# Kernel tuning notes

Hardware: AMD Instinct MI355X
Metric: run time of the kernel (lower is better)

The kernel has to match this reference:

```python
import jax, jax.numpy as jnp
import numpy as np


def _skew(p):
    # p: (...,3) -> (...,3,3) skew-symmetric matrices
    x, y, z = p[..., 0], p[..., 1], p[..., 2]
    o = jnp.zeros_like(x)
    return jnp.stack([
        jnp.stack([o, -z, y], -1),
        jnp.stack([z, o, -x], -1),
        jnp.stack([-y, x, o], -1)], -2)


def _so3exp(w):
    # Rodrigues formula for a single (3,) rotation vector
    theta = jnp.linalg.norm(w)
    small = theta < 1e-7
    th = jnp.where(small, 1.0, theta)
    W = _skew(w)
    A = jnp.where(small, 1.0, jnp.sin(th) / th)
    B = jnp.where(small, 0.5, (1.0 - jnp.cos(th)) / (th * th))
    return jnp.eye(3, dtype=w.dtype) + A * W + B * (W @ W)


def setup_inputs() -> dict:
    key = jax.random.key(0)
    k1, k2, k3, k4, k5, k6 = jax.random.split(key, 6)
    N, C, H, W = 100000, 128, 480, 640
    xy = jax.random.uniform(k1, (N, 2), minval=-1.0, maxval=1.0)
    z = jax.random.uniform(k2, (N, 1), minval=4.0, maxval=8.0)
    pts3D = jnp.concatenate([xy, z], -1).astype(jnp.float32)
    feature_ref = jax.random.normal(k3, (N, C), dtype=jnp.float32)
    feature_map_query = jax.random.normal(k4, (C, H, W), dtype=jnp.float32)
    feature_grad_x = jax.random.normal(k5, (C, H, W), dtype=jnp.float32) * 0.1
    feature_grad_y = jax.random.normal(k6, (C, H, W), dtype=jnp.float32) * 0.1
    K = jnp.array([[400.0, 0.0, 320.0], [0.0, 400.0, 200.0], [0.0, 0.0, 1.0]], dtype=jnp.float32)
    return {"pts3D": pts3D, "feature_ref": feature_ref,
            "feature_map_query": feature_map_query,
            "feature_grad_x": feature_grad_x, "feature_grad_y": feature_grad_y,
            "K": K, "n_iters": 5}


def reference(pts3D, feature_ref, feature_map_query, feature_grad_x, feature_grad_y, K, n_iters):
    C, H, W = feature_map_query.shape
    N = pts3D.shape[0]

    def gather(fm, ii, jj):
        return fm[:, ii, jj].T  # (N, C)

    def project(Rm, tv):
        p = pts3D @ Rm.T + tv                       # (N,3) points in camera frame
        uv = p @ K.T
        proj = jnp.round(uv[:, :2] / uv[:, 2:3]).astype(jnp.int32) - 1  # (N,2) [x,y]
        ii = jnp.clip(proj[:, 1], 0, H - 1)          # row (flip)
        jj = jnp.clip(proj[:, 0], 0, W - 1)          # col
        return p, ii, jj

    def step(carry, i):
        R, t, lam, lr, prev_cost = carry
        p, ii, jj = project(R, t)
        error = gather(feature_map_query, ii, jj) - feature_ref  # (N,C)
        cost_mean = (0.5 * (error ** 2).sum(-1)).mean()
        prev_cost = jnp.where(i == 0, cost_mean, prev_cost)
        eye = jnp.broadcast_to(jnp.eye(3, dtype=p.dtype), (N, 3, 3))
        J_p_T = jnp.concatenate([eye, -_skew(p)], -1)            # (N,3,6)
        fx, fy = K[0, 0], K[1, 1]
        x, y, z = p[:, 0], p[:, 1], p[:, 2]
        o = jnp.ones_like(z); zz = jnp.zeros_like(z)
        J_px_p = jnp.stack([fx * o, zz, -fx * x / z, zz, fy * o, -fy * y / z], -1)
        J_px_p = J_px_p.reshape(N, 2, 3) / z[:, None, None]       # (N,2,3)
        gx = gather(feature_grad_x, ii, jj)
        gy = gather(feature_grad_y, ii, jj)
        J_f_px = jnp.stack([gx, gy], -1)                          # (N,C,2)
        J = jnp.einsum('ncp,npq,nqk->nck', J_f_px, J_px_p, J_p_T)  # (N,C,6)
        g = jnp.einsum('nck,nc->k', J, error)                     # (6,)
        Hess = jnp.einsum('nci,ncj->ij', J, J)                    # (6,6)
        Hd = Hess + jnp.diag(jnp.diagonal(Hess) + 1e-9) * lam     # LM damping
        delta = -lr * jnp.linalg.solve(Hd, g)
        dt, dw = delta[:3], delta[3:6]
        dR = _so3exp(dw)
        R_new = dR @ R
        t_new = dR @ t + dt
        _, ii2, jj2 = project(R_new, t_new)
        new_error = gather(feature_map_query, ii2, jj2) - feature_ref
        new_cost = (0.5 * (new_error ** 2).sum(-1)).mean()
        worse = new_cost > prev_cost
        lam = jnp.clip(lam * jnp.where(worse, 10.0, 0.1), 1e-6, 1e4)
        lr = jnp.where(worse, jnp.clip(0.1 * lr, 1e-3, 1.0), 0.1)
        R = jnp.where(worse, R, R_new)
        t = jnp.where(worse, t, t_new)
        prev_cost = jnp.where(worse, prev_cost, new_cost)
        return (R, t, lam, lr, prev_cost), None

    R0 = jnp.eye(3, dtype=pts3D.dtype)
    t0 = jnp.array([1.0, 1.0, 0.0], dtype=pts3D.dtype)
    init = (R0, t0, jnp.float32(0.01), jnp.float32(0.1), jnp.float32(0.0))
    (R, t, _, _, _), _ = jax.lax.scan(step, init, jnp.arange(n_iters))
    return R, t
```

## Files before the change

### kernel.cpp

```cpp
#include <hip/hip_runtime.h>

#define NPTS 100000
#define CCH  128
#define HIMG 480
#define WIMG 640
#define HWSZ (HIMG*WIMG)
#define TROW 384
#define NSLOT 8

struct State {
  double slotsA[NSLOT][28];
  double slotsC[NSLOT][28];
  double accA[28];
  double accB;
  double prev_cost;
  float R[9];
  float t[3];
  float Rc[9];
  float tc[3];
  float lam;
  float lr;
};

__device__ State g_st;

#define HIDX(i,j) (6 + (6*(i)) - ((i)*((i)-1))/2 + ((j)-(i)))

__device__ __forceinline__ float sel6(int k, float a0,float a1,float a2,float a3,float a4,float a5){
  float r = a0;
  r = (k==1)?a1:r; r = (k==2)?a2:r; r = (k==3)?a3:r; r = (k==4)?a4:r; r = (k==5)?a5:r;
  return r;
}

#define TP_PIX 32
#define NTILE (HWSZ/TP_PIX)
#define TIX(p,c) ((p)*132 + ((c) ^ ((((p)>>2)&3)<<3)))

__global__ __launch_bounds__(256) void k_transpose(
    const float* __restrict__ Q, const float* __restrict__ GX,
    const float* __restrict__ GY, float* __restrict__ T)
{
  if(blockIdx.x==0 && threadIdx.x==0){
    for(int s=0;s<NSLOT;s++) for(int k=0;k<28;k++){ g_st.slotsA[s][k]=0.0; g_st.slotsC[s][k]=0.0; }
    g_st.prev_cost=0.0;
    g_st.R[0]=1.f; g_st.R[1]=0.f; g_st.R[2]=0.f;
    g_st.R[3]=0.f; g_st.R[4]=1.f; g_st.R[5]=0.f;
    g_st.R[6]=0.f; g_st.R[7]=0.f; g_st.R[8]=1.f;
    g_st.t[0]=1.f; g_st.t[1]=1.f; g_st.t[2]=0.f;
    g_st.lam=0.01f; g_st.lr=0.1f;
  }

  __shared__ float tile[TP_PIX*132];
  const int bid = blockIdx.x;
  const int m   = bid / NTILE;
  const int tl  = bid - m*NTILE;
  const int pbase = tl*TP_PIX;
  const float* __restrict__ src = (m==0)?Q:((m==1)?GX:GY);
  const int t = threadIdx.x;

  const int c_lo = t>>3;
  const int p4   = (t&7)<<2;
  #pragma unroll
  for(int k=0;k<4;k++){
    const int c = c_lo + 32*k;
    const float4 v = *reinterpret_cast<const float4*>(src + (size_t)c*HWSZ + pbase + p4);
    tile[TIX(p4+0,c)] = v.x;
    tile[TIX(p4+1,c)] = v.y;
    tile[TIX(p4+2,c)] = v.z;
    tile[TIX(p4+3,c)] = v.w;
  }
  __syncthreads();
  const int p = t>>3;
  const int a = t&7;
  float* dstp = T + (size_t)(pbase+p)*TROW + m*128;
  #pragma unroll
  for(int q=0;q<4;q++){
    const int ch = a*4 + 32*q;
    const float4 v = *reinterpret_cast<const float4*>(&tile[TIX(p,ch)]);
    *reinterpret_cast<float4*>(dstp + ch) = v;
  }
}

__global__ __launch_bounds__(256) void k_pass(
    const float* __restrict__ pts, const float* __restrict__ ref,
    const float* __restrict__ T,   const float* __restrict__ Kin, int cand)
{
  __shared__ double wacc[4][28];
  const int lane = threadIdx.x & 63;
  const int wid  = threadIdx.x >> 6;

  const float fx=Kin[0], cx=Kin[2], fy=Kin[4], cy=Kin[5];
  const float* Rp = cand ? g_st.Rc : g_st.R;
  const float* tp = cand ? g_st.tc : g_st.t;
  const float R00=Rp[0],R01=Rp[1],R02=Rp[2];
  const float R10=Rp[3],R11=Rp[4],R12=Rp[5];
  const float R20=Rp[6],R21=Rp[7],R22=Rp[8];
  const float t0=tp[0],t1=tp[1],t2=tp[2];

  float a[28];
  #pragma unroll
  for(int k=0;k<28;k++) a[k]=0.f;

  const int c0 = lane*2;
  const int wstride = gridDim.x*4;
  for(int n = blockIdx.x*4 + wid; n < NPTS; n += wstride){
    const float X=pts[3*n], Y=pts[3*n+1], Z=pts[3*n+2];
    const float x = R00*X + R01*Y + R02*Z + t0;
    const float y = R10*X + R11*Y + R12*Z + t1;
    const float z = R20*X + R21*Y + R22*Z + t2;
    const float uu = fx*x + cx*z;
    const float vv = fy*y + cy*z;
    const int pjx = (int)rintf(uu/z) - 1;
    const int pjy = (int)rintf(vv/z) - 1;
    const int jj = pjx<0?0:(pjx>(WIMG-1)?(WIMG-1):pjx);
    const int ii = pjy<0?0:(pjy>(HIMG-1)?(HIMG-1):pjy);
    const int idx = ii*WIMG + jj;

    const float* base = T + (size_t)idx*TROW + c0;
    const float2 qq = *reinterpret_cast<const float2*>(base);
    const float2 gg = *reinterpret_cast<const float2*>(base + 128);
    const float2 hh = *reinterpret_cast<const float2*>(base + 256);
    const float2 rr = *reinterpret_cast<const float2*>(ref + n*CCH + c0);
    const float e0 = qq.x-rr.x, e1 = qq.y-rr.y;

    const float see = e0*e0 + e1*e1;
    const float sb1 = gg.x*e0 + gg.y*e1;
    const float sb2 = hh.x*e0 + hh.y*e1;
    const float sa11= gg.x*gg.x + gg.y*gg.y;
    const float sa12= gg.x*hh.x + gg.y*hh.y;
    const float sa22= hh.x*hh.x + hh.y*hh.y;

    const float iz = 1.0f/z;
    const float ux = x*iz, vy = y*iz;
    float M0[6], M1[6];
    M0[0]=fx*iz; M0[1]=0.f;   M0[2]=-fx*ux*iz; M0[3]=-fx*ux*vy;       M0[4]=fx*(1.f+ux*ux); M0[5]=-fx*vy;
    M1[0]=0.f;   M1[1]=fy*iz; M1[2]=-fy*vy*iz; M1[3]=-fy*(1.f+vy*vy); M1[4]=fy*ux*vy;       M1[5]=fy*ux;

    #pragma unroll
    for(int i=0;i<6;i++) a[i] += M0[i]*sb1 + M1[i]*sb2;
    #pragma unroll
    for(int i=0;i<6;i++){
      #pragma unroll
      for(int j=i;j<6;j++){
        a[HIDX(i,j)] += sa11*(M0[i]*M0[j]) + sa12*(M0[i]*M1[j]+M1[i]*M0[j]) + sa22*(M1[i]*M1[j]);
      }
    }
    a[27] += see;
  }

  #pragma unroll
  for(int k=0;k<28;k++){
    double v = (double)a[k];
    #pragma unroll
    for(int m=1;m<64;m<<=1) v += __shfl_xor(v,m);
    if(lane==0) wacc[wid][k]=v;
  }
  __syncthreads();
  if(threadIdx.x<28){
    double s = wacc[0][threadIdx.x]+wacc[1][threadIdx.x]+wacc[2][threadIdx.x]+wacc[3][threadIdx.x];
    double* slot = cand ? g_st.slotsC[blockIdx.x & (NSLOT-1)] : g_st.slotsA[blockIdx.x & (NSLOT-1)];
    atomicAdd(&slot[threadIdx.x], s);
  }
}

__global__ void k_step(int iter){
  __shared__ double red[28];
  __shared__ double sC[28];
  const int t = threadIdx.x;
  if(t<28){
    double c=0.0, aa=0.0;
    for(int s=0;s<NSLOT;s++){ c += g_st.slotsC[s][t]; aa += g_st.slotsA[s][t]; }
    sC[t]=c; red[t]=aa;
  }
  __syncthreads();
  if(t!=0) return;

  if(iter>0){
    const double new_cost = 0.5*sC[27]/(double)NPTS;
    const bool worse = new_cost > g_st.prev_cost;
    float lam = g_st.lam * (worse?10.0f:0.1f);
    g_st.lam = fminf(fmaxf(lam,1e-6f),10000.0f);
    g_st.lr  = worse ? fminf(fmaxf(0.1f*g_st.lr,0.001f),1.0f) : 0.1f;
    if(!worse){
      for(int k=0;k<28;k++){
        red[k]=sC[k];
        g_st.slotsA[0][k]=sC[k];
        for(int s=1;s<NSLOT;s++) g_st.slotsA[s][k]=0.0;
      }
      for(int i=0;i<9;i++) g_st.R[i]=g_st.Rc[i];
      for(int i=0;i<3;i++) g_st.t[i]=g_st.tc[i];
      g_st.prev_cost = new_cost;
    }
    for(int s=0;s<NSLOT;s++) for(int k=0;k<28;k++) g_st.slotsC[s][k]=0.0;
  } else {
    g_st.prev_cost = 0.5*red[27]/(double)NPTS;
  }

  const double lam = (double)g_st.lam;
  double Hm[6][6];
  int m=0;
  for(int i=0;i<6;i++) for(int j=i;j<6;j++){ double v=red[6+m]; m++; Hm[i][j]=v; Hm[j][i]=v; }
  double A[6][7];
  for(int i=0;i<6;i++){
    for(int j=0;j<6;j++) A[i][j]=Hm[i][j];
    A[i][i] = Hm[i][i] + lam*(Hm[i][i]+1e-9);
    A[i][6] = red[i];
  }
  for(int k=0;k<6;k++){
    int piv=k; double mx=fabs(A[k][k]);
    for(int r=k+1;r<6;r++){ double v=fabs(A[r][k]); if(v>mx){mx=v;piv=r;} }
    if(piv!=k){ for(int c=k;c<7;c++){ double tmp=A[k][c]; A[k][c]=A[piv][c]; A[piv][c]=tmp; } }
    const double inv = 1.0/A[k][k];
    for(int r=k+1;r<6;r++){
      const double f = A[r][k]*inv;
      for(int c=k;c<7;c++) A[r][c] -= f*A[k][c];
    }
  }
  double xsol[6];
  for(int r=5;r>=0;r--){
    double s=A[r][6];
    for(int c=r+1;c<6;c++) s -= A[r][c]*xsol[c];
    xsol[r]=s/A[r][r];
  }
  const double lr = (double)g_st.lr;
  float d[6];
  for(int k=0;k<6;k++) d[k] = (float)(-lr*xsol[k]);

  const float wx=d[3], wy=d[4], wz=d[5];
  const float th2 = wx*wx+wy*wy+wz*wz;
  const float theta = sqrtf(th2);
  const bool small = theta < 1e-7f;
  const float th = small?1.0f:theta;
  const float Aa = small?1.0f:(sinf(th)/th);
  const float Bb = small?0.5f:((1.0f-cosf(th))/(th*th));
  float Wm[3][3] = {{0.f,-wz,wy},{wz,0.f,-wx},{-wy,wx,0.f}};
  float W2[3][3];
  for(int i=0;i<3;i++) for(int j=0;j<3;j++)
    W2[i][j] = Wm[i][0]*Wm[0][j] + Wm[i][1]*Wm[1][j] + Wm[i][2]*Wm[2][j];
  float dR[3][3];
  for(int i=0;i<3;i++) for(int j=0;j<3;j++)
    dR[i][j] = (i==j?1.f:0.f) + Aa*Wm[i][j] + Bb*W2[i][j];

  float Rn[9], tn[3];
  for(int i=0;i<3;i++){
    for(int j=0;j<3;j++)
      Rn[i*3+j] = dR[i][0]*g_st.R[0*3+j] + dR[i][1]*g_st.R[1*3+j] + dR[i][2]*g_st.R[2*3+j];
    tn[i] = dR[i][0]*g_st.t[0] + dR[i][1]*g_st.t[1] + dR[i][2]*g_st.t[2] + d[i];
  }
  for(int i=0;i<9;i++) g_st.Rc[i]=Rn[i];
  for(int i=0;i<3;i++) g_st.tc[i]=tn[i];
}

__global__ void k_finish(float* __restrict__ out, int out_size){
  const int t = threadIdx.x;
  if(t==0){
    double c=0.0; for(int s=0;s<NSLOT;s++) c += g_st.slotsC[s][27];
    const double new_cost = 0.5*c/(double)NPTS;
    if(!(new_cost > g_st.prev_cost)){
      for(int i=0;i<9;i++) g_st.R[i]=g_st.Rc[i];
      for(int i=0;i<3;i++) g_st.t[i]=g_st.tc[i];
    }
  }
  __syncthreads();
  if(t<9 && t<out_size) out[t]=g_st.R[t];
  else if(t<12 && t<out_size) out[t]=g_st.t[t-9];
}

__global__ void k_init(){
  if(threadIdx.x==0){
    for(int i=0;i<28;i++) g_st.accA[i]=0.0;
    g_st.accB=0.0; g_st.prev_cost=0.0;
    g_st.R[0]=1.f; g_st.R[1]=0.f; g_st.R[2]=0.f;
    g_st.R[3]=0.f; g_st.R[4]=1.f; g_st.R[5]=0.f;
    g_st.R[6]=0.f; g_st.R[7]=0.f; g_st.R[8]=1.f;
    g_st.t[0]=1.f; g_st.t[1]=1.f; g_st.t[2]=0.f;
    g_st.lam=0.01f; g_st.lr=0.1f;
  }
}

__global__ __launch_bounds__(256) void k_accum(
    const float* __restrict__ pts, const float* __restrict__ ref,
    const float* __restrict__ Q,   const float* __restrict__ GX,
    const float* __restrict__ GY,  const float* __restrict__ Kin)
{
  __shared__ double wacc[4][28];
  const int lane = threadIdx.x & 63;
  const int wid  = threadIdx.x >> 6;

  const float fx=Kin[0], cx=Kin[2], fy=Kin[4], cy=Kin[5];
  const float R00=g_st.R[0],R01=g_st.R[1],R02=g_st.R[2];
  const float R10=g_st.R[3],R11=g_st.R[4],R12=g_st.R[5];
  const float R20=g_st.R[6],R21=g_st.R[7],R22=g_st.R[8];
  const float t0=g_st.t[0],t1=g_st.t[1],t2=g_st.t[2];

  int role = 3, ci = 0, cj = 0;
  if(lane < 6){ role = 0; ci = lane; cj = lane; }
  else if(lane < 27){
    role = 1;
    const int tt = lane - 6;
    int i = 5;
    i = (tt < 20) ? 4 : i;
    i = (tt < 18) ? 3 : i;
    i = (tt < 15) ? 2 : i;
    i = (tt < 11) ? 1 : i;
    i = (tt <  6) ? 0 : i;
    const int rs = (i==0)?0:(i==1)?6:(i==2)?11:(i==3)?15:(i==4)?18:20;
    ci = i; cj = i + (tt - rs);
  }
  else if(lane == 27){ role = 2; }

  double acc = 0.0;
  const int c0 = lane*2;
  const int wstride = gridDim.x*4;
  for(int n = blockIdx.x*4 + wid; n < NPTS; n += wstride){
    const float X=pts[3*n], Y=pts[3*n+1], Z=pts[3*n+2];
    const float x = R00*X + R01*Y + R02*Z + t0;
    const float y = R10*X + R11*Y + R12*Z + t1;
    const float z = R20*X + R21*Y + R22*Z + t2;
    const float uu = fx*x + cx*z;
    const float vv = fy*y + cy*z;
    const int pjx = (int)rintf(uu/z) - 1;
    const int pjy = (int)rintf(vv/z) - 1;
    const int jj = pjx<0?0:(pjx>(WIMG-1)?(WIMG-1):pjx);
    const int ii = pjy<0?0:(pjy>(HIMG-1)?(HIMG-1):pjy);
    const int idx = ii*WIMG + jj;

    const int o0 = c0*HWSZ + idx;
    const float q0 = Q[o0],  q1 = Q[o0+HWSZ];
    const float gx0= GX[o0], gx1= GX[o0+HWSZ];
    const float gy0= GY[o0], gy1= GY[o0+HWSZ];
    const float2 rr = *reinterpret_cast<const float2*>(ref + n*CCH + c0);
    const float e0 = q0-rr.x, e1 = q1-rr.y;

    float see = e0*e0 + e1*e1;
    float sb1 = gx0*e0 + gx1*e1;
    float sb2 = gy0*e0 + gy1*e1;
    float sa11= gx0*gx0 + gx1*gx1;
    float sa12= gx0*gy0 + gx1*gy1;
    float sa22= gy0*gy0 + gy1*gy1;
    #pragma unroll
    for(int m=1;m<64;m<<=1){
      see += __shfl_xor(see,m);
      sb1 += __shfl_xor(sb1,m);
      sb2 += __shfl_xor(sb2,m);
      sa11+= __shfl_xor(sa11,m);
      sa12+= __shfl_xor(sa12,m);
      sa22+= __shfl_xor(sa22,m);
    }

    const float iz = 1.0f/z;
    const float ux = x*iz, vy = y*iz;
    const float m00=fx*iz, m01=0.f,    m02=-fx*ux*iz, m03=-fx*ux*vy,       m04=fx*(1.f+ux*ux), m05=-fx*vy;
    const float m10=0.f,   m11=fy*iz,  m12=-fy*vy*iz, m13=-fy*(1.f+vy*vy), m14=fy*ux*vy,       m15=fy*ux;

    float contrib;
    if(role==0){
      const float M0=sel6(ci,m00,m01,m02,m03,m04,m05);
      const float M1=sel6(ci,m10,m11,m12,m13,m14,m15);
      contrib = M0*sb1 + M1*sb2;
    } else if(role==1){
      const float M0i=sel6(ci,m00,m01,m02,m03,m04,m05);
      const float M1i=sel6(ci,m10,m11,m12,m13,m14,m15);
      const float M0j=sel6(cj,m00,m01,m02,m03,m04,m05);
      const float M1j=sel6(cj,m10,m11,m12,m13,m14,m15);
      contrib = sa11*(M0i*M0j) + sa12*(M0i*M1j + M1i*M0j) + sa22*(M1i*M1j);
    } else if(role==2){
      contrib = see;
    } else {
      contrib = 0.f;
    }
    acc += (double)contrib;
  }

  if(lane<28) wacc[wid][lane] = acc;
  __syncthreads();
  if(threadIdx.x<28){
    double s = wacc[0][threadIdx.x]+wacc[1][threadIdx.x]+wacc[2][threadIdx.x]+wacc[3][threadIdx.x];
    atomicAdd(&g_st.accA[threadIdx.x], s);
  }
}

__global__ __launch_bounds__(256) void k_cost(
    const float* __restrict__ pts, const float* __restrict__ ref,
    const float* __restrict__ Q,   const float* __restrict__ Kin)
{
  __shared__ double wacc[4];
  const int lane = threadIdx.x & 63;
  const int wid  = threadIdx.x >> 6;

  const float fx=Kin[0], cx=Kin[2], fy=Kin[4], cy=Kin[5];
  const float R00=g_st.Rc[0],R01=g_st.Rc[1],R02=g_st.Rc[2];
  const float R10=g_st.Rc[3],R11=g_st.Rc[4],R12=g_st.Rc[5];
  const float R20=g_st.Rc[6],R21=g_st.Rc[7],R22=g_st.Rc[8];
  const float t0=g_st.tc[0],t1=g_st.tc[1],t2=g_st.tc[2];

  double acc = 0.0;
  const int c0 = lane*2;
  const int wstride = gridDim.x*4;
  for(int n = blockIdx.x*4 + wid; n < NPTS; n += wstride){
    const float X=pts[3*n], Y=pts[3*n+1], Z=pts[3*n+2];
    const float x = R00*X + R01*Y + R02*Z + t0;
    const float y = R10*X + R11*Y + R12*Z + t1;
    const float z = R20*X + R21*Y + R22*Z + t2;
    const float uu = fx*x + cx*z;
    const float vv = fy*y + cy*z;
    const int pjx = (int)rintf(uu/z) - 1;
    const int pjy = (int)rintf(vv/z) - 1;
    const int jj = pjx<0?0:(pjx>(WIMG-1)?(WIMG-1):pjx);
    const int ii = pjy<0?0:(pjy>(HIMG-1)?(HIMG-1):pjy);
    const int idx = ii*WIMG + jj;

    const int o0 = c0*HWSZ + idx;
    const float q0 = Q[o0], q1 = Q[o0+HWSZ];
    const float2 rr = *reinterpret_cast<const float2*>(ref + n*CCH + c0);
    const float e0 = q0-rr.x, e1 = q1-rr.y;
    float see = e0*e0 + e1*e1;
    #pragma unroll
    for(int m=1;m<64;m<<=1) see += __shfl_xor(see,m);
    if(lane==0) acc += (double)see;
  }
  if(lane==0) wacc[wid]=acc;
  __syncthreads();
  if(threadIdx.x==0) atomicAdd(&g_st.accB, wacc[0]+wacc[1]+wacc[2]+wacc[3]);
}

__global__ void k_solve(int iter){
  if(threadIdx.x!=0) return;
  const double cost_mean = 0.5*g_st.accA[27]/(double)NPTS;
  if(iter==0) g_st.prev_cost = cost_mean;
  const double lam = (double)g_st.lam;

  double Hm[6][6];
  int m=0;
  for(int i=0;i<6;i++) for(int j=i;j<6;j++){ double v=g_st.accA[6+m]; m++; Hm[i][j]=v; Hm[j][i]=v; }
  double A[6][7];
  for(int i=0;i<6;i++){
    for(int j=0;j<6;j++) A[i][j]=Hm[i][j];
    A[i][i] = Hm[i][i] + lam*(Hm[i][i]+1e-9);
    A[i][6] = g_st.accA[i];
  }
  for(int k=0;k<6;k++){
    int piv=k; double mx=fabs(A[k][k]);
    for(int r=k+1;r<6;r++){ double v=fabs(A[r][k]); if(v>mx){mx=v;piv=r;} }
    if(piv!=k){ for(int c=k;c<7;c++){ double tmp=A[k][c]; A[k][c]=A[piv][c]; A[piv][c]=tmp; } }
    const double inv = 1.0/A[k][k];
    for(int r=k+1;r<6;r++){
      const double f = A[r][k]*inv;
      for(int c=k;c<7;c++) A[r][c] -= f*A[k][c];
    }
  }
  double xsol[6];
  for(int r=5;r>=0;r--){
    double s=A[r][6];
    for(int c=r+1;c<6;c++) s -= A[r][c]*xsol[c];
    xsol[r]=s/A[r][r];
  }
  const double lr = (double)g_st.lr;
  float d[6];
  for(int k=0;k<6;k++) d[k] = (float)(-lr*xsol[k]);

  const float wx=d[3], wy=d[4], wz=d[5];
  const float th2 = wx*wx+wy*wy+wz*wz;
  const float theta = sqrtf(th2);
  const bool small = theta < 1e-7f;
  const float th = small?1.0f:theta;
  const float Aa = small?1.0f:(sinf(th)/th);
  const float Bb = small?0.5f:((1.0f-cosf(th))/(th*th));
  float Wm[3][3] = {{0.f,-wz,wy},{wz,0.f,-wx},{-wy,wx,0.f}};
  float W2[3][3];
  for(int i=0;i<3;i++) for(int j=0;j<3;j++)
    W2[i][j] = Wm[i][0]*Wm[0][j] + Wm[i][1]*Wm[1][j] + Wm[i][2]*Wm[2][j];
  float dR[3][3];
  for(int i=0;i<3;i++) for(int j=0;j<3;j++)
    dR[i][j] = (i==j?1.f:0.f) + Aa*Wm[i][j] + Bb*W2[i][j];

  float Rn[9], tn[3];
  for(int i=0;i<3;i++){
    for(int j=0;j<3;j++)
      Rn[i*3+j] = dR[i][0]*g_st.R[0*3+j] + dR[i][1]*g_st.R[1*3+j] + dR[i][2]*g_st.R[2*3+j];
    tn[i] = dR[i][0]*g_st.t[0] + dR[i][1]*g_st.t[1] + dR[i][2]*g_st.t[2] + d[i];
  }
  for(int i=0;i<9;i++) g_st.Rc[i]=Rn[i];
  for(int i=0;i<3;i++) g_st.tc[i]=tn[i];
  g_st.accB = 0.0;
}

__global__ void k_update(){
  if(threadIdx.x!=0) return;
  const double new_cost = 0.5*g_st.accB/(double)NPTS;
  const bool worse = new_cost > g_st.prev_cost;
  float lam = g_st.lam * (worse?10.0f:0.1f);
  lam = fminf(fmaxf(lam,1e-6f),10000.0f);
  g_st.lam = lam;
  g_st.lr  = worse ? fminf(fmaxf(0.1f*g_st.lr,0.001f),1.0f) : 0.1f;
  if(!worse){
    for(int i=0;i<9;i++) g_st.R[i]=g_st.Rc[i];
    for(int i=0;i<3;i++) g_st.t[i]=g_st.tc[i];
    g_st.prev_cost = new_cost;
  }
  for(int i=0;i<28;i++) g_st.accA[i]=0.0;
}

__global__ void k_write(float* __restrict__ out, int out_size){
  const int i = threadIdx.x;
  if(i<9 && i<out_size) out[i]=g_st.R[i];
  else if(i<12 && i<out_size) out[i]=g_st.t[i-9];
}

extern "C" void kernel_launch(void* const* d_in, const int* in_sizes, int n_in,
                              void* d_out, int out_size, void* d_ws, size_t ws_size,
                              hipStream_t stream) {
  const float* pts = (const float*)d_in[0];
  const float* ref = (const float*)d_in[1];
  const float* Q   = (const float*)d_in[2];
  const float* GX  = (const float*)d_in[3];
  const float* GY  = (const float*)d_in[4];
  const float* Km  = (const float*)d_in[5];
  float* out = (float*)d_out;

  const size_t need = (size_t)HWSZ * TROW * sizeof(float);
  const int GRID = 2048;

  if(d_ws != nullptr && ws_size >= need){
    float* T = (float*)d_ws;
    k_transpose<<<3*NTILE,256,0,stream>>>(Q,GX,GY,T);
    k_pass<<<GRID,256,0,stream>>>(pts,ref,T,Km,0);
    for(int i=0;i<5;i++){
      k_step<<<1,64,0,stream>>>(i);
      k_pass<<<GRID,256,0,stream>>>(pts,ref,T,Km,1);
    }
    k_finish<<<1,64,0,stream>>>(out,out_size);
  } else {
    k_init<<<1,64,0,stream>>>();
    for(int i=0;i<5;i++){
      k_accum<<<GRID,256,0,stream>>>(pts,ref,Q,GX,GY,Km);
      k_solve<<<1,64,0,stream>>>(i);
      k_cost<<<GRID,256,0,stream>>>(pts,ref,Q,Km);
      k_update<<<1,64,0,stream>>>();
    }
    k_write<<<1,64,0,stream>>>(out,out_size);
  }
}
```

Measured before the change: 998.0 us.

## Interleave query and gradient channels per pixel and process two points per wave

The transposed feature table now interleaves value, x-gradient and y-gradient in groups of four channels per pixel. Each half-wave handles one point with float4 loads, so a wave covers two points at once. The transpose kernel now handles all three maps in one block with a padded, swizzled shared tile. The Hessian accumulation is rewritten with shared partial products that skip the structural zeros. This targets fewer and wider memory transactions in the gather-heavy pass, in exchange for a larger shared tile and more registers.

```diff
diff --git a/kernel.cpp b/kernel.cpp
--- a/kernel.cpp
+++ b/kernel.cpp
@@ -34,7 +34,8 @@
 
 #define TP_PIX 32
 #define NTILE (HWSZ/TP_PIX)
-#define TIX(p,c) ((p)*132 + ((c) ^ ((((p)>>2)&3)<<3)))
+#define TROWP 392
+#define TIX(p,fo) ((p)*TROWP + ((fo) ^ ((((p)>>2)&3)<<2)))
 
 __global__ __launch_bounds__(256) void k_transpose(
     const float* __restrict__ Q, const float* __restrict__ GX,
@@ -50,34 +51,33 @@
     g_st.lam=0.01f; g_st.lr=0.1f;
   }
 
-  __shared__ float tile[TP_PIX*132];
-  const int bid = blockIdx.x;
-  const int m   = bid / NTILE;
-  const int tl  = bid - m*NTILE;
-  const int pbase = tl*TP_PIX;
-  const float* __restrict__ src = (m==0)?Q:((m==1)?GX:GY);
+  __shared__ __align__(16) float tile[TP_PIX*TROWP];
+  const int pbase = blockIdx.x * TP_PIX;
   const int t = threadIdx.x;
 
   const int c_lo = t>>3;
-  const int p4   = (t&7)<<2;
+  const int px4  = (t&7)<<2;
   #pragma unroll
-  for(int k=0;k<4;k++){
-    const int c = c_lo + 32*k;
-    const float4 v = *reinterpret_cast<const float4*>(src + (size_t)c*HWSZ + pbase + p4);
-    tile[TIX(p4+0,c)] = v.x;
-    tile[TIX(p4+1,c)] = v.y;
-    tile[TIX(p4+2,c)] = v.z;
-    tile[TIX(p4+3,c)] = v.w;
+  for(int j=0;j<12;j++){
+    const int m = j>>2;
+    const float* __restrict__ src = (m==0)?Q:((m==1)?GX:GY);
+    const int c = c_lo + 32*(j&3);
+    const float4 v = *reinterpret_cast<const float4*>(src + (size_t)c*HWSZ + pbase + px4);
+    const int fo = 12*(c>>2) + 4*m + (c&3);
+    tile[TIX(px4+0,fo)] = v.x;
+    tile[TIX(px4+1,fo)] = v.y;
+    tile[TIX(px4+2,fo)] = v.z;
+    tile[TIX(px4+3,fo)] = v.w;
   }
   __syncthreads();
   const int p = t>>3;
-  const int a = t&7;
-  float* dstp = T + (size_t)(pbase+p)*TROW + m*128;
+  const int s = t&7;
+  float* dstp = T + (size_t)(pbase+p)*TROW;
   #pragma unroll
-  for(int q=0;q<4;q++){
-    const int ch = a*4 + 32*q;
-    const float4 v = *reinterpret_cast<const float4*>(&tile[TIX(p,ch)]);
-    *reinterpret_cast<float4*>(dstp + ch) = v;
+  for(int j=0;j<12;j++){
+    const int fo = 4*(s + 8*j);
+    const float4 v = *reinterpret_cast<const float4*>(&tile[TIX(p,fo)]);
+    *reinterpret_cast<float4*>(dstp + fo) = v;
   }
 }
 
@@ -88,6 +88,8 @@
   __shared__ double wacc[4][28];
   const int lane = threadIdx.x & 63;
   const int wid  = threadIdx.x >> 6;
+  const int h = lane >> 5;
+  const int l = lane & 31;
 
   const float fx=Kin[0], cx=Kin[2], fy=Kin[4], cy=Kin[5];
   const float* Rp = cand ? g_st.Rc : g_st.R;
@@ -101,9 +103,10 @@
   #pragma unroll
   for(int k=0;k<28;k++) a[k]=0.f;
 
-  const int c0 = lane*2;
+  const int NPAIR = NPTS/2;
   const int wstride = gridDim.x*4;
-  for(int n = blockIdx.x*4 + wid; n < NPTS; n += wstride){
+  for(int pp = blockIdx.x*4 + wid; pp < NPAIR; pp += wstride){
+    const int n = 2*pp + h;
     const float X=pts[3*n], Y=pts[3*n+1], Z=pts[3*n+2];
     const float x = R00*X + R01*Y + R02*Z + t0;
     const float y = R10*X + R11*Y + R12*Z + t1;
@@ -116,35 +119,66 @@
     const int ii = pjy<0?0:(pjy>(HIMG-1)?(HIMG-1):pjy);
     const int idx = ii*WIMG + jj;
 
-    const float* base = T + (size_t)idx*TROW + c0;
-    const float2 qq = *reinterpret_cast<const float2*>(base);
-    const float2 gg = *reinterpret_cast<const float2*>(base + 128);
-    const float2 hh = *reinterpret_cast<const float2*>(base + 256);
-    const float2 rr = *reinterpret_cast<const float2*>(ref + n*CCH + c0);
-    const float e0 = qq.x-rr.x, e1 = qq.y-rr.y;
-
-    const float see = e0*e0 + e1*e1;
-    const float sb1 = gg.x*e0 + gg.y*e1;
-    const float sb2 = hh.x*e0 + hh.y*e1;
-    const float sa11= gg.x*gg.x + gg.y*gg.y;
-    const float sa12= gg.x*hh.x + gg.y*hh.y;
-    const float sa22= hh.x*hh.x + hh.y*hh.y;
+    const float* base = T + (size_t)idx*TROW + 12*l;
+    const float4 qq = *reinterpret_cast<const float4*>(base);
+    const float4 gx = *reinterpret_cast<const float4*>(base+4);
+    const float4 gy = *reinterpret_cast<const float4*>(base+8);
+    const float4 rr = *reinterpret_cast<const float4*>(ref + (size_t)n*CCH + 4*l);
+
+    const float e0=qq.x-rr.x, e1=qq.y-rr.y, e2=qq.z-rr.z, e3=qq.w-rr.w;
+    const float see = e0*e0+e1*e1+e2*e2+e3*e3;
+    const float sb1 = gx.x*e0+gx.y*e1+gx.z*e2+gx.w*e3;
+    const float sb2 = gy.x*e0+gy.y*e1+gy.z*e2+gy.w*e3;
+    const float sa11= gx.x*gx.x+gx.y*gx.y+gx.z*gx.z+gx.w*gx.w;
+    const float sa12= gx.x*gy.x+gx.y*gy.y+gx.z*gy.z+gx.w*gy.w;
+    const float sa22= gy.x*gy.x+gy.y*gy.y+gy.z*gy.z+gy.w*gy.w;
 
     const float iz = 1.0f/z;
     const float ux = x*iz, vy = y*iz;
-    float M0[6], M1[6];
-    M0[0]=fx*iz; M0[1]=0.f;   M0[2]=-fx*ux*iz; M0[3]=-fx*ux*vy;       M0[4]=fx*(1.f+ux*ux); M0[5]=-fx*vy;
-    M1[0]=0.f;   M1[1]=fy*iz; M1[2]=-fy*vy*iz; M1[3]=-fy*(1.f+vy*vy); M1[4]=fy*ux*vy;       M1[5]=fy*ux;
-
-    #pragma unroll
-    for(int i=0;i<6;i++) a[i] += M0[i]*sb1 + M1[i]*sb2;
-    #pragma unroll
-    for(int i=0;i<6;i++){
-      #pragma unroll
-      for(int j=i;j<6;j++){
-        a[HIDX(i,j)] += sa11*(M0[i]*M0[j]) + sa12*(M0[i]*M1[j]+M1[i]*M0[j]) + sa22*(M1[i]*M1[j]);
-      }
-    }
+    const float m00=fx*iz,  m02=-fx*ux*iz, m03=-fx*ux*vy,       m04=fx*(1.f+ux*ux), m05=-fx*vy;
+    const float m11=fy*iz,  m12=-fy*vy*iz, m13=-fy*(1.f+vy*vy), m14=fy*ux*vy,       m15=fy*ux;
+
+    a[0] += m00*sb1;
+    a[1] += m11*sb2;
+    a[2] += m02*sb1 + m12*sb2;
+    a[3] += m03*sb1 + m13*sb2;
+    a[4] += m04*sb1 + m14*sb2;
+    a[5] += m05*sb1 + m15*sb2;
+
+    const float p00 = sa11*m00;
+    const float p10 = sa12*m00;
+    const float p01 = sa12*m11;
+    const float p11 = sa22*m11;
+    const float p02 = sa11*m02 + sa12*m12;
+    const float p12 = sa12*m02 + sa22*m12;
+    const float p03 = sa11*m03 + sa12*m13;
+    const float p13 = sa12*m03 + sa22*m13;
+    const float p04 = sa11*m04 + sa12*m14;
+    const float p14 = sa12*m04 + sa22*m14;
+    const float p05 = sa11*m05 + sa12*m15;
+    const float p15 = sa12*m05 + sa22*m15;
+
+    a[HIDX(0,0)] += p00*m00;
+    a[HIDX(0,1)] += p10*m11;
+    a[HIDX(0,2)] += p00*m02 + p10*m12;
+    a[HIDX(0,3)] += p00*m03 + p10*m13;
+    a[HIDX(0,4)] += p00*m04 + p10*m14;
+    a[HIDX(0,5)] += p00*m05 + p10*m15;
+    a[HIDX(1,1)] += p11*m11;
+    a[HIDX(1,2)] += p01*m02 + p11*m12;
+    a[HIDX(1,3)] += p01*m03 + p11*m13;
+    a[HIDX(1,4)] += p01*m04 + p11*m14;
+    a[HIDX(1,5)] += p01*m05 + p11*m15;
+    a[HIDX(2,2)] += p02*m02 + p12*m12;
+    a[HIDX(2,3)] += p02*m03 + p12*m13;
+    a[HIDX(2,4)] += p02*m04 + p12*m14;
+    a[HIDX(2,5)] += p02*m05 + p12*m15;
+    a[HIDX(3,3)] += p03*m03 + p13*m13;
+    a[HIDX(3,4)] += p03*m04 + p13*m14;
+    a[HIDX(3,5)] += p03*m05 + p13*m15;
+    a[HIDX(4,4)] += p04*m04 + p14*m14;
+    a[HIDX(4,5)] += p04*m05 + p14*m15;
+    a[HIDX(5,5)] += p05*m05 + p15*m15;
     a[27] += see;
   }
 
@@ -523,7 +557,7 @@
 
   if(d_ws != nullptr && ws_size >= need){
     float* T = (float*)d_ws;
-    k_transpose<<<3*NTILE,256,0,stream>>>(Q,GX,GY,T);
+    k_transpose<<<NTILE,256,0,stream>>>(Q,GX,GY,T);
     k_pass<<<GRID,256,0,stream>>>(pts,ref,T,Km,0);
     for(int i=0;i<5;i++){
       k_step<<<1,64,0,stream>>>(i);
```

Result: faster. 865.5 us (-13.3%).
